# Optimization experiments

Hardware: AMD Instinct MI355X
Metric: run time of the kernel (lower is better)

Reference implementation:

```python
import jax, jax.numpy as jnp
import numpy as np

TEMPERATURE = 0.1


def setup_inputs() -> dict:
    key = jax.random.key(0)
    k1, k2 = jax.random.split(key)
    B, B_pos, D = 8192, 8192, 1024
    generated = jax.random.normal(k1, (B, D), dtype=jnp.float32)
    positive = jax.random.normal(k2, (B_pos, D), dtype=jnp.float32)
    return {"generated": generated, "positive": positive}


def _pairwise_dist_sq(x, y):
    # (N, M) squared L2 distances, clamped at 0
    x_norm = jnp.sum(x * x, axis=-1, keepdims=True)          # (N, 1)
    y_norm = jnp.sum(y * y, axis=-1, keepdims=True)          # (M, 1)
    d2 = x_norm + y_norm.T - 2.0 * (x @ y.T)
    return jnp.clip(d2, 0.0)


def reference(generated, positive):
    gen = generated.reshape(generated.shape[0], -1)
    pos = positive.reshape(positive.shape[0], -1)
    B = gen.shape[0]

    # Attraction: softmax over distances to positives.
    dist_pos = jnp.sqrt(_pairwise_dist_sq(gen, pos))          # (B, B_pos)
    w_pos = jax.nn.softmax(-dist_pos / TEMPERATURE, axis=1)
    # sum_j w_ij (pos_j - gen_i) == (w_pos @ pos) - gen  (rows of w sum to 1)
    attraction = w_pos @ pos - gen                            # (B, D)

    # Repulsion: softmax over distances to other generated samples (diag masked).
    d2_neg = _pairwise_dist_sq(gen, gen)
    eye = jnp.eye(B, dtype=bool)
    dist_neg = jnp.sqrt(jnp.where(eye, jnp.inf, d2_neg))      # inf diag -> weight 0
    w_neg = jax.nn.softmax(-dist_neg / TEMPERATURE, axis=1)
    repulsion = w_neg @ gen - gen                             # (B, D)

    drift = attraction - repulsion
    target = jax.lax.stop_gradient(gen + drift)
    loss = jnp.mean((gen - target) ** 2)

    drift_norm = jnp.mean(jnp.linalg.norm(drift, axis=-1))
    attraction_norm = jnp.mean(jnp.linalg.norm(attraction, axis=-1))
    repulsion_norm = jnp.mean(jnp.linalg.norm(repulsion, axis=-1))
    return (loss, drift_norm, attraction_norm, repulsion_norm)
```

## Files before the change

### kernel.cpp

```cpp
#include <hip/hip_runtime.h>
#include <stdint.h>

#define INV_T 10.0f
#define SHIFT_ 460.0f
#define MROWS 8192
#define DDIM 1024
#define CHUNK 1024

typedef __attribute__((ext_vector_type(8))) short bf16x8;
typedef __attribute__((ext_vector_type(4))) float f32x4;

__device__ __forceinline__ float bf2f(unsigned short u) {
  return __uint_as_float(((unsigned int)u) << 16);
}
__device__ __forceinline__ unsigned short f2bf(float f) {
  unsigned int u = __float_as_uint(f);
  return (unsigned short)((u + 0x7FFFu + ((u >> 16) & 1u)) >> 16);
}
__device__ __forceinline__ void gl2lds16(const unsigned short* g, unsigned short* l) {
  __builtin_amdgcn_global_load_lds((const __attribute__((address_space(1))) void*)g,
                                   (__attribute__((address_space(3))) void*)l, 16, 0, 0);
}

__global__ void prepT_kernel(const float* __restrict__ gen, const float* __restrict__ pos,
                             unsigned short* __restrict__ gen_h, unsigned short* __restrict__ pos_h,
                             unsigned short* __restrict__ genT, unsigned short* __restrict__ posT,
                             float* __restrict__ gn2, float* __restrict__ pn2) {
  __shared__ float tile[64][65];
  __shared__ float psum[64][4];
  int b = blockIdx.x;
  const float* src; unsigned short* dstT; unsigned short* dstH; float* n2;
  if (b < 2048) { src = gen; dstT = genT; dstH = gen_h; n2 = gn2; }
  else          { src = pos; dstT = posT; dstH = pos_h; n2 = pn2; b -= 2048; }
  int tj = b >> 4, td = b & 15;
  int t = threadIdx.x;
#pragma unroll
  for (int it = 0; it < 16; ++it) {
    int idx = it * 256 + t;
    int r = idx >> 6, c = idx & 63;
    tile[r][c] = src[(size_t)(tj * 64 + r) * DDIM + td * 64 + c];
  }
  __syncthreads();
  {
    int r4 = t >> 2, q = t & 3;
    float s = 0.f;
#pragma unroll
    for (int i = 0; i < 16; ++i) { float v = tile[r4][q * 16 + i]; s += v * v; }
    psum[r4][q] = s;
  }
#pragma unroll
  for (int it = 0; it < 16; ++it) {
    int idx = it * 256 + t;
    int r = idx >> 6, c = idx & 63;
    dstH[(size_t)(tj * 64 + r) * DDIM + td * 64 + c] = f2bf(tile[r][c]);
  }
#pragma unroll
  for (int it = 0; it < 16; ++it) {
    int idx = it * 256 + t;
    int d = idx >> 6, j = idx & 63;
    dstT[(size_t)(td * 64 + d) * MROWS + tj * 64 + j] = f2bf(tile[j][d]);
  }
  __syncthreads();
  if (t < 64) {
    float s = psum[t][0] + psum[t][1] + psum[t][2] + psum[t][3];
    atomicAdd(&n2[tj * 64 + t], s);
  }
}

__launch_bounds__(256, 2)
__global__ void gemm_sc2(const unsigned short* __restrict__ Aq,
                         const unsigned short* __restrict__ Bpos,
                         const unsigned short* __restrict__ Bgen,
                         int j0lo, int j0hi,
                         unsigned short* __restrict__ PaLo, unsigned short* __restrict__ PrLo,
                         unsigned short* __restrict__ PaHi, unsigned short* __restrict__ PrHi,
                         const float* __restrict__ gn2, const float* __restrict__ pn2,
                         float* __restrict__ lsumA, float* __restrict__ lsumR) {
  __shared__ __align__(16) unsigned short Al[128 * 64];
  __shared__ __align__(16) unsigned short Bl[128 * 64];

  const int orig = blockIdx.x + 64 * (blockIdx.y + 16 * blockIdx.z);
  const int wid = (orig & 7) * 256 + (orig >> 3);
  const int gy = wid & 15;
  const int bx = (wid >> 4) & 63;
  const int z = wid >> 10;
  const int hi = gy >> 3;
  const int by = gy & 7;

  const int j0 = hi ? j0hi : j0lo;
  const unsigned short* B = z ? Bgen : Bpos;
  const float* kn2 = z ? gn2 : pn2;
  float* lsum = z ? lsumR : lsumA;
  unsigned short* Pout = hi ? (z ? PrHi : PaHi) : (z ? PrLo : PaLo);

  const int t = threadIdx.x;
  const int w = t >> 6, lane = t & 63, l15 = lane & 15, quad = lane >> 4;
  const int wm = w >> 1, wn = w & 1;
  const long m0 = (long)bx * 128;
  const long n0 = (long)by * 128;
  const int trow = t >> 3;
  const int tcol = (((t & 7) ^ (trow & 7)) * 8);

  f32x4 acc[4][4];
#pragma unroll
  for (int i = 0; i < 4; ++i)
#pragma unroll
    for (int j = 0; j < 4; ++j) acc[i][j] = (f32x4){0.f, 0.f, 0.f, 0.f};

  const unsigned short* Ab = Aq + (m0 + trow) * DDIM + tcol;
  const unsigned short* Bb = B + ((long)j0 + n0 + trow) * DDIM + tcol;
  unsigned short* Alw = Al + t * 8;
  unsigned short* Blw = Bl + t * 8;
  const int ue = (quad ^ (l15 & 7)) * 8;

  for (int ks = 0; ks < DDIM / 64; ++ks) {
    const long ko = (long)ks * 64;
#pragma unroll
    for (int i = 0; i < 4; ++i) gl2lds16(Ab + (long)i * 32 * DDIM + ko, Alw + i * 2048);
#pragma unroll
    for (int i = 0; i < 4; ++i) gl2lds16(Bb + (long)i * 32 * DDIM + ko, Blw + i * 2048);
    __syncthreads();
#pragma unroll
    for (int kk = 0; kk < 2; ++kk) {
      const int uo = ue ^ (kk * 32);
      bf16x8 af[4], bfr[4];
#pragma unroll
      for (int mi = 0; mi < 4; ++mi)
        af[mi] = *(const bf16x8*)(Al + (wm * 64 + mi * 16 + l15) * 64 + uo);
#pragma unroll
      for (int ni = 0; ni < 4; ++ni)
        bfr[ni] = *(const bf16x8*)(Bl + (wn * 64 + ni * 16 + l15) * 64 + uo);
#pragma unroll
      for (int mi = 0; mi < 4; ++mi)
#pragma unroll
        for (int ni = 0; ni < 4; ++ni)
          acc[mi][ni] = __builtin_amdgcn_mfma_f32_16x16x32_bf16(af[mi], bfr[ni], acc[mi][ni], 0, 0, 0);
    }
    __syncthreads();
  }

#pragma unroll
  for (int mi = 0; mi < 4; ++mi) {
    float rs[4] = {0.f, 0.f, 0.f, 0.f};
#pragma unroll
    for (int ni = 0; ni < 4; ++ni) {
      int c = (int)n0 + wn * 64 + ni * 16 + l15;
      float kn = kn2[j0 + c];
#pragma unroll
      for (int reg = 0; reg < 4; ++reg) {
        long r = m0 + wm * 64 + mi * 16 + quad * 4 + reg;
        float v = acc[mi][ni][reg];
        float d2 = gn2[r] + kn - 2.0f * v;
        float p = __expf(SHIFT_ - INV_T * sqrtf(fmaxf(d2, 0.0f)));
        if (z && (int)r == (j0 + c)) p = 0.0f;
        rs[reg] += p;
        Pout[r * (long)CHUNK + c] = f2bf(p);
      }
    }
#pragma unroll
    for (int reg = 0; reg < 4; ++reg) {
      float v = rs[reg];
      v += __shfl_xor(v, 1); v += __shfl_xor(v, 2);
      v += __shfl_xor(v, 4); v += __shfl_xor(v, 8);
      if (l15 == 0) atomicAdd(&lsum[m0 + wm * 64 + mi * 16 + quad * 4 + reg], v);
    }
  }
}

#define KSEG(Abase, Bbase, LDA_, LDB_)                                                     \
  {                                                                                        \
    const unsigned short* Ab_ = (Abase) + (m0 + trow) * (LDA_) + tcol;                     \
    const unsigned short* Bb_ = (Bbase) + (n0 + trow) * (LDB_) + tcol;                     \
    for (int ks = 0; ks < 16; ++ks) {                                                      \
      const long ko = (long)ks * 64;                                                       \
      _Pragma("unroll")                                                                    \
      for (int i = 0; i < 4; ++i) gl2lds16(Ab_ + (long)i * 32 * (LDA_) + ko, Alw + i * 2048); \
      _Pragma("unroll")                                                                    \
      for (int i = 0; i < 4; ++i) gl2lds16(Bb_ + (long)i * 32 * (LDB_) + ko, Blw + i * 2048); \
      __syncthreads();                                                                     \
      _Pragma("unroll")                                                                    \
      for (int kk = 0; kk < 2; ++kk) {                                                     \
        const int uo = ue ^ (kk * 32);                                                     \
        bf16x8 af[4], bfr[4];                                                              \
        _Pragma("unroll")                                                                  \
        for (int mi = 0; mi < 4; ++mi)                                                     \
          af[mi] = *(const bf16x8*)(Al + (wm * 64 + mi * 16 + l15) * 64 + uo);             \
        _Pragma("unroll")                                                                  \
        for (int ni = 0; ni < 4; ++ni)                                                     \
          bfr[ni] = *(const bf16x8*)(Bl + (wn * 64 + ni * 16 + l15) * 64 + uo);            \
        _Pragma("unroll")                                                                  \
        for (int mi = 0; mi < 4; ++mi)                                                     \
          _Pragma("unroll")                                                                \
          for (int ni = 0; ni < 4; ++ni)                                                   \
            acc[mi][ni] = __builtin_amdgcn_mfma_f32_16x16x32_bf16(af[mi], bfr[ni], acc[mi][ni], 0, 0, 0); \
      }                                                                                    \
      __syncthreads();                                                                     \
    }                                                                                      \
  }

__launch_bounds__(256, 2)
__global__ void gemm_pv(const unsigned short* __restrict__ Pa0, const unsigned short* __restrict__ Pr0,
                        const unsigned short* __restrict__ Pa1, const unsigned short* __restrict__ Pr1,
                        const unsigned short* __restrict__ Pa2, const unsigned short* __restrict__ Pr2,
                        const unsigned short* __restrict__ Pa3, const unsigned short* __restrict__ Pr3,
                        const unsigned short* __restrict__ Va0, const unsigned short* __restrict__ Vr0,
                        const unsigned short* __restrict__ Va1, const unsigned short* __restrict__ Vr1,
                        const unsigned short* __restrict__ Va2, const unsigned short* __restrict__ Vr2,
                        const unsigned short* __restrict__ Va3, const unsigned short* __restrict__ Vr3,
                        unsigned short* __restrict__ OA, unsigned short* __restrict__ OR_,
                        int first) {
  __shared__ __align__(16) unsigned short Al[128 * 64];
  __shared__ __align__(16) unsigned short Bl[128 * 64];

  const int orig = blockIdx.x + 64 * (blockIdx.y + 8 * blockIdx.z);
  const int wid = (orig & 7) * 128 + (orig >> 3);
  const int by = wid & 7;
  const int bx = (wid >> 3) & 63;
  const int z = wid >> 9;

  const unsigned short* A0 = z ? Pr0 : Pa0;
  const unsigned short* B0 = z ? Vr0 : Va0;
  const unsigned short* A1 = z ? Pr1 : Pa1;
  const unsigned short* B1 = z ? Vr1 : Va1;
  const unsigned short* A2 = z ? Pr2 : Pa2;
  const unsigned short* B2 = z ? Vr2 : Va2;
  const unsigned short* A3 = z ? Pr3 : Pa3;
  const unsigned short* B3 = z ? Vr3 : Va3;

  const int t = threadIdx.x;
  const int w = t >> 6, lane = t & 63, l15 = lane & 15, quad = lane >> 4;
  const int wm = w >> 1, wn = w & 1;
  const long m0 = (long)bx * 128;
  const long n0 = (long)by * 128;
  const int trow = t >> 3;
  const int tcol = (((t & 7) ^ (trow & 7)) * 8);

  f32x4 acc[4][4];
#pragma unroll
  for (int i = 0; i < 4; ++i)
#pragma unroll
    for (int j = 0; j < 4; ++j) acc[i][j] = (f32x4){0.f, 0.f, 0.f, 0.f};

  unsigned short* Alw = Al + t * 8;
  unsigned short* Blw = Bl + t * 8;
  const int ue = (quad ^ (l15 & 7)) * 8;

  KSEG(A0, B0, CHUNK, MROWS);
  KSEG(A1, B1, CHUNK, MROWS);
  KSEG(A2, B2, CHUNK, MROWS);
  KSEG(A3, B3, CHUNK, MROWS);

  unsigned short* Oh = z ? OR_ : OA;
#pragma unroll
  for (int mi = 0; mi < 4; ++mi)
#pragma unroll
    for (int ni = 0; ni < 4; ++ni) {
      long c = n0 + wn * 64 + ni * 16 + l15;
#pragma unroll
      for (int reg = 0; reg < 4; ++reg) {
        long r = m0 + wm * 64 + mi * 16 + quad * 4 + reg;
        long off = r * DDIM + c;
        float v = acc[mi][ni][reg];
        Oh[off] = f2bf(first ? v : (bf2f(Oh[off]) + v));
      }
    }
}
#undef KSEG

__global__ void epi_kernel(const unsigned short* __restrict__ OA, const unsigned short* __restrict__ OR_,
                           const float* __restrict__ lsumA, const float* __restrict__ lsumR,
                           const float* __restrict__ genf, float* __restrict__ gs) {
  __shared__ float wsL[4], wsD[4], wsA[4], wsR[4];
  const int t = threadIdx.x;
  const int w = t >> 6;
  const int lane = t & 63;
  float accL = 0.f, accD = 0.f, accA = 0.f, accR = 0.f;

  for (int i = 0; i < 8; ++i) {
    const int row = blockIdx.x * 32 + w * 8 + i;
    const float invlA = 1.0f / lsumA[row];
    const float invlR = 1.0f / lsumR[row];
    float ssA = 0.f, ssR = 0.f, ssD = 0.f;
#pragma unroll
    for (int u = 0; u < 4; ++u) {
      const long off = (long)row * DDIM + u * 256 + lane * 4;
      float4 g = *(const float4*)(genf + off);
      ushort4 oa = *(const ushort4*)(OA + off);
      ushort4 orr = *(const ushort4*)(OR_ + off);
      float g4[4] = {g.x, g.y, g.z, g.w};
      float a4[4] = {bf2f(oa.x), bf2f(oa.y), bf2f(oa.z), bf2f(oa.w)};
      float r4[4] = {bf2f(orr.x), bf2f(orr.y), bf2f(orr.z), bf2f(orr.w)};
#pragma unroll
      for (int e = 0; e < 4; ++e) {
        float a_ = a4[e] * invlA - g4[e];
        float r_ = r4[e] * invlR - g4[e];
        float d_ = a_ - r_;
        ssA += a_ * a_; ssR += r_ * r_; ssD += d_ * d_;
      }
    }
#pragma unroll
    for (int m = 1; m < 64; m <<= 1) {
      ssA += __shfl_xor(ssA, m);
      ssR += __shfl_xor(ssR, m);
      ssD += __shfl_xor(ssD, m);
    }
    accA += sqrtf(ssA); accR += sqrtf(ssR); accD += sqrtf(ssD); accL += ssD;
  }
  if (lane == 0) { wsL[w] = accL; wsD[w] = accD; wsA[w] = accA; wsR[w] = accR; }
  __syncthreads();
  if (t == 0) {
    atomicAdd(&gs[0], wsL[0] + wsL[1] + wsL[2] + wsL[3]);
    atomicAdd(&gs[1], wsD[0] + wsD[1] + wsD[2] + wsD[3]);
    atomicAdd(&gs[2], wsA[0] + wsA[1] + wsA[2] + wsA[3]);
    atomicAdd(&gs[3], wsR[0] + wsR[1] + wsR[2] + wsR[3]);
  }
}

__global__ void finalize_kernel(const float* __restrict__ gs, float* __restrict__ out) {
  int t = threadIdx.x;
  if (t == 0) out[0] = gs[0] / (8192.0f * 1024.0f);
  if (t == 1) out[1] = gs[1] / 8192.0f;
  if (t == 2) out[2] = gs[2] / 8192.0f;
  if (t == 3) out[3] = gs[3] / 8192.0f;
}

extern "C" void kernel_launch(void* const* d_in, const int* in_sizes, int n_in,
                              void* d_out, int out_size, void* d_ws, size_t ws_size,
                              hipStream_t stream) {
  const float* gen = (const float*)d_in[0];
  const float* pos = (const float*)d_in[1];
  char* ws = (char*)d_ws;
  const size_t MB = (size_t)1 << 20;

  unsigned short* gen_h = (unsigned short*)(ws + 0 * MB);
  unsigned short* pos_h = (unsigned short*)(ws + 16 * MB);
  unsigned short* genT  = (unsigned short*)(ws + 32 * MB);
  unsigned short* posT  = (unsigned short*)(ws + 48 * MB);
  unsigned short* Pa[4] = {(unsigned short*)(ws + 64 * MB),  (unsigned short*)(ws + 96 * MB),
                           (unsigned short*)(ws + 128 * MB), (unsigned short*)(ws + 160 * MB)};
  unsigned short* Pr[4] = {(unsigned short*)(ws + 80 * MB),  (unsigned short*)(ws + 112 * MB),
                           (unsigned short*)(ws + 144 * MB), (unsigned short*)(ws + 176 * MB)};
  unsigned short* OhA = (unsigned short*)(ws + 192 * MB);
  unsigned short* OhR = (unsigned short*)(ws + 208 * MB);
  float* gn2   = (float*)(ws + 224 * MB);
  float* pn2   = (float*)(ws + 224 * MB + 32768);
  float* lsumA = (float*)(ws + 224 * MB + 65536);
  float* lsumR = (float*)(ws + 224 * MB + 98304);
  float* gs    = (float*)(ws + 224 * MB + 131072);

  hipMemsetAsync(gn2, 0, 131072 + 16, stream);
  prepT_kernel<<<dim3(4096), dim3(256), 0, stream>>>(gen, pos, gen_h, pos_h, genT, posT, gn2, pn2);

  for (int p = 0; p < 2; ++p) {
    const int c0 = 4 * p;
    gemm_sc2<<<dim3(64, 16, 2), dim3(256), 0, stream>>>(
        gen_h, pos_h, gen_h, c0 * CHUNK, (c0 + 1) * CHUNK,
        Pa[0], Pr[0], Pa[1], Pr[1], gn2, pn2, lsumA, lsumR);
    gemm_sc2<<<dim3(64, 16, 2), dim3(256), 0, stream>>>(
        gen_h, pos_h, gen_h, (c0 + 2) * CHUNK, (c0 + 3) * CHUNK,
        Pa[2], Pr[2], Pa[3], Pr[3], gn2, pn2, lsumA, lsumR);
    const long j0 = (long)c0 * CHUNK;
    gemm_pv<<<dim3(64, 8, 2), dim3(256), 0, stream>>>(
        Pa[0], Pr[0], Pa[1], Pr[1], Pa[2], Pr[2], Pa[3], Pr[3],
        posT + j0, genT + j0, posT + j0 + CHUNK, genT + j0 + CHUNK,
        posT + j0 + 2 * CHUNK, genT + j0 + 2 * CHUNK, posT + j0 + 3 * CHUNK, genT + j0 + 3 * CHUNK,
        OhA, OhR, p == 0);
  }

  epi_kernel<<<dim3(256), dim3(256), 0, stream>>>(OhA, OhR, lsumA, lsumR, gen, gs);
  finalize_kernel<<<dim3(1), dim3(64), 0, stream>>>(gs, (float*)d_out);
}
```

Before: 760.3 us.

## Exploit symmetry of repulsion distance matrix with triangular tile scoring

```diff
diff --git a/kernel.cpp b/kernel.cpp
--- a/kernel.cpp
+++ b/kernel.cpp
@@ -68,6 +68,216 @@
 }
 
 __launch_bounds__(256, 2)
+__global__ void repsc_tri(const unsigned short* __restrict__ Ah,
+                          unsigned short* __restrict__ Prep,
+                          const float* __restrict__ gn2,
+                          float* __restrict__ lsumR) {
+  __shared__ __align__(16) unsigned short lbuf[128 * 132];
+  unsigned short* Al = lbuf;
+  unsigned short* Bl = lbuf + 128 * 64;
+
+  const int orig = blockIdx.x;
+  const int wid = (orig & 7) * 260 + (orig >> 3);
+  int r = (int)((sqrtf(8.0f * (float)wid + 1.0f) - 1.0f) * 0.5f);
+  while ((r + 1) * (r + 2) / 2 <= wid) ++r;
+  while (r * (r + 1) / 2 > wid) --r;
+  const int c = wid - r * (r + 1) / 2;
+
+  const int t = threadIdx.x;
+  const int w = t >> 6, lane = t & 63, l15 = lane & 15, quad = lane >> 4;
+  const int wm = w >> 1, wn = w & 1;
+  const long m0 = (long)r * 128;
+  const long n0 = (long)c * 128;
+  const int trow = t >> 3;
+  const int tcol = (((t & 7) ^ (trow & 7)) * 8);
+
+  f32x4 acc[4][4];
+#pragma unroll
+  for (int i = 0; i < 4; ++i)
+#pragma unroll
+    for (int j = 0; j < 4; ++j) acc[i][j] = (f32x4){0.f, 0.f, 0.f, 0.f};
+
+  const unsigned short* Ab = Ah + (m0 + trow) * DDIM + tcol;
+  const unsigned short* Bb = Ah + (n0 + trow) * DDIM + tcol;
+  unsigned short* Alw = Al + t * 8;
+  unsigned short* Blw = Bl + t * 8;
+  const int ue = (quad ^ (l15 & 7)) * 8;
+
+  for (int ks = 0; ks < DDIM / 64; ++ks) {
+    const long ko = (long)ks * 64;
+#pragma unroll
+    for (int i = 0; i < 4; ++i) gl2lds16(Ab + (long)i * 32 * DDIM + ko, Alw + i * 2048);
+#pragma unroll
+    for (int i = 0; i < 4; ++i) gl2lds16(Bb + (long)i * 32 * DDIM + ko, Blw + i * 2048);
+    __syncthreads();
+#pragma unroll
+    for (int kk = 0; kk < 2; ++kk) {
+      const int uo = ue ^ (kk * 32);
+      bf16x8 af[4], bfr[4];
+#pragma unroll
+      for (int mi = 0; mi < 4; ++mi)
+        af[mi] = *(const bf16x8*)(Al + (wm * 64 + mi * 16 + l15) * 64 + uo);
+#pragma unroll
+      for (int ni = 0; ni < 4; ++ni)
+        bfr[ni] = *(const bf16x8*)(Bl + (wn * 64 + ni * 16 + l15) * 64 + uo);
+#pragma unroll
+      for (int mi = 0; mi < 4; ++mi)
+#pragma unroll
+        for (int ni = 0; ni < 4; ++ni)
+          acc[mi][ni] = __builtin_amdgcn_mfma_f32_16x16x32_bf16(af[mi], bfr[ni], acc[mi][ni], 0, 0, 0);
+    }
+    __syncthreads();
+  }
+
+  const bool offd = (r != c);
+  float cs[4] = {0.f, 0.f, 0.f, 0.f};
+#pragma unroll
+  for (int mi = 0; mi < 4; ++mi) {
+    float rs[4] = {0.f, 0.f, 0.f, 0.f};
+#pragma unroll
+    for (int ni = 0; ni < 4; ++ni) {
+      const int colL = wn * 64 + ni * 16 + l15;
+      const long col = n0 + colL;
+      float kn = gn2[col];
+#pragma unroll
+      for (int reg = 0; reg < 4; ++reg) {
+        const int rowL = wm * 64 + mi * 16 + quad * 4 + reg;
+        const long row = m0 + rowL;
+        float v = acc[mi][ni][reg];
+        float d2 = gn2[row] + kn - 2.0f * v;
+        float p = __expf(SHIFT_ - INV_T * sqrtf(fmaxf(d2, 0.0f)));
+        if (row == col) p = 0.0f;
+        rs[reg] += p;
+        cs[ni] += p;
+        unsigned short pb = f2bf(p);
+        Prep[row * (long)MROWS + col] = pb;
+        if (offd) lbuf[rowL * 132 + colL] = pb;
+      }
+    }
+#pragma unroll
+    for (int reg = 0; reg < 4; ++reg) {
+      float v = rs[reg];
+      v += __shfl_xor(v, 1); v += __shfl_xor(v, 2);
+      v += __shfl_xor(v, 4); v += __shfl_xor(v, 8);
+      if (l15 == 0) atomicAdd(&lsumR[m0 + wm * 64 + mi * 16 + quad * 4 + reg], v);
+    }
+  }
+  if (offd) {
+#pragma unroll
+    for (int ni = 0; ni < 4; ++ni) {
+      float v = cs[ni];
+      v += __shfl_xor(v, 16); v += __shfl_xor(v, 32);
+      if (quad == 0) atomicAdd(&lsumR[n0 + wn * 64 + ni * 16 + l15], v);
+    }
+    __syncthreads();
+#pragma unroll
+    for (int it = 0; it < 16; ++it) {
+      int lin = it * 256 + t;
+      int i = lin >> 5, jg = lin & 31, j = jg * 4;
+      ushort4 o;
+      o.x = lbuf[(j + 0) * 132 + i];
+      o.y = lbuf[(j + 1) * 132 + i];
+      o.z = lbuf[(j + 2) * 132 + i];
+      o.w = lbuf[(j + 3) * 132 + i];
+      *(ushort4*)(Prep + (n0 + i) * (long)MROWS + m0 + j) = o;
+    }
+  }
+}
+
+__launch_bounds__(256, 2)
+__global__ void gemm_sca(const unsigned short* __restrict__ Aq,
+                         const unsigned short* __restrict__ Bpos,
+                         int j0lo, int j0hi,
+                         unsigned short* __restrict__ PaLo, unsigned short* __restrict__ PaHi,
+                         const float* __restrict__ gn2, const float* __restrict__ pn2,
+                         float* __restrict__ lsumA) {
+  __shared__ __align__(16) unsigned short Al[128 * 64];
+  __shared__ __align__(16) unsigned short Bl[128 * 64];
+
+  const int orig = blockIdx.x + 64 * blockIdx.y;
+  const int wid = (orig & 7) * 128 + (orig >> 3);
+  const int gy = wid & 15;
+  const int bx = (wid >> 4) & 63;
+  const int hi = gy >> 3;
+  const int by = gy & 7;
+
+  const int j0 = hi ? j0hi : j0lo;
+  unsigned short* Pout = hi ? PaHi : PaLo;
+
+  const int t = threadIdx.x;
+  const int w = t >> 6, lane = t & 63, l15 = lane & 15, quad = lane >> 4;
+  const int wm = w >> 1, wn = w & 1;
+  const long m0 = (long)bx * 128;
+  const long n0 = (long)by * 128;
+  const int trow = t >> 3;
+  const int tcol = (((t & 7) ^ (trow & 7)) * 8);
+
+  f32x4 acc[4][4];
+#pragma unroll
+  for (int i = 0; i < 4; ++i)
+#pragma unroll
+    for (int j = 0; j < 4; ++j) acc[i][j] = (f32x4){0.f, 0.f, 0.f, 0.f};
+
+  const unsigned short* Ab = Aq + (m0 + trow) * DDIM + tcol;
+  const unsigned short* Bb = Bpos + ((long)j0 + n0 + trow) * DDIM + tcol;
+  unsigned short* Alw = Al + t * 8;
+  unsigned short* Blw = Bl + t * 8;
+  const int ue = (quad ^ (l15 & 7)) * 8;
+
+  for (int ks = 0; ks < DDIM / 64; ++ks) {
+    const long ko = (long)ks * 64;
+#pragma unroll
+    for (int i = 0; i < 4; ++i) gl2lds16(Ab + (long)i * 32 * DDIM + ko, Alw + i * 2048);
+#pragma unroll
+    for (int i = 0; i < 4; ++i) gl2lds16(Bb + (long)i * 32 * DDIM + ko, Blw + i * 2048);
+    __syncthreads();
+#pragma unroll
+    for (int kk = 0; kk < 2; ++kk) {
+      const int uo = ue ^ (kk * 32);
+      bf16x8 af[4], bfr[4];
+#pragma unroll
+      for (int mi = 0; mi < 4; ++mi)
+        af[mi] = *(const bf16x8*)(Al + (wm * 64 + mi * 16 + l15) * 64 + uo);
+#pragma unroll
+      for (int ni = 0; ni < 4; ++ni)
+        bfr[ni] = *(const bf16x8*)(Bl + (wn * 64 + ni * 16 + l15) * 64 + uo);
+#pragma unroll
+      for (int mi = 0; mi < 4; ++mi)
+#pragma unroll
+        for (int ni = 0; ni < 4; ++ni)
+          acc[mi][ni] = __builtin_amdgcn_mfma_f32_16x16x32_bf16(af[mi], bfr[ni], acc[mi][ni], 0, 0, 0);
+    }
+    __syncthreads();
+  }
+
+#pragma unroll
+  for (int mi = 0; mi < 4; ++mi) {
+    float rs[4] = {0.f, 0.f, 0.f, 0.f};
+#pragma unroll
+    for (int ni = 0; ni < 4; ++ni) {
+      int cc = (int)n0 + wn * 64 + ni * 16 + l15;
+      float kn = pn2[j0 + cc];
+#pragma unroll
+      for (int reg = 0; reg < 4; ++reg) {
+        long rr = m0 + wm * 64 + mi * 16 + quad * 4 + reg;
+        float v = acc[mi][ni][reg];
+        float d2 = gn2[rr] + kn - 2.0f * v;
+        float p = __expf(SHIFT_ - INV_T * sqrtf(fmaxf(d2, 0.0f)));
+        rs[reg] += p;
+        Pout[rr * (long)CHUNK + cc] = f2bf(p);
+      }
+    }
+#pragma unroll
+    for (int reg = 0; reg < 4; ++reg) {
+      float v = rs[reg];
+      v += __shfl_xor(v, 1); v += __shfl_xor(v, 2);
+      v += __shfl_xor(v, 4); v += __shfl_xor(v, 8);
+      if (l15 == 0) atomicAdd(&lsumA[m0 + wm * 64 + mi * 16 + quad * 4 + reg], v);
+    }
+  }
+}
+
+__launch_bounds__(256, 2)
 __global__ void gemm_sc2(const unsigned short* __restrict__ Aq,
                          const unsigned short* __restrict__ Bpos,
                          const unsigned short* __restrict__ Bgen,
@@ -144,17 +354,17 @@
     float rs[4] = {0.f, 0.f, 0.f, 0.f};
 #pragma unroll
     for (int ni = 0; ni < 4; ++ni) {
-      int c = (int)n0 + wn * 64 + ni * 16 + l15;
-      float kn = kn2[j0 + c];
+      int cc = (int)n0 + wn * 64 + ni * 16 + l15;
+      float kn = kn2[j0 + cc];
 #pragma unroll
       for (int reg = 0; reg < 4; ++reg) {
-        long r = m0 + wm * 64 + mi * 16 + quad * 4 + reg;
+        long rr = m0 + wm * 64 + mi * 16 + quad * 4 + reg;
         float v = acc[mi][ni][reg];
-        float d2 = gn2[r] + kn - 2.0f * v;
+        float d2 = gn2[rr] + kn - 2.0f * v;
         float p = __expf(SHIFT_ - INV_T * sqrtf(fmaxf(d2, 0.0f)));
-        if (z && (int)r == (j0 + c)) p = 0.0f;
+        if (z && (int)rr == (j0 + cc)) p = 0.0f;
         rs[reg] += p;
-        Pout[r * (long)CHUNK + c] = f2bf(p);
+        Pout[rr * (long)CHUNK + cc] = f2bf(p);
       }
     }
 #pragma unroll
@@ -167,16 +377,16 @@
   }
 }
 
-#define KSEG(Abase, Bbase, LDA_, LDB_)                                                     \
+#define KSEG(Abase, LDA_, Bbase)                                                           \
   {                                                                                        \
     const unsigned short* Ab_ = (Abase) + (m0 + trow) * (LDA_) + tcol;                     \
-    const unsigned short* Bb_ = (Bbase) + (n0 + trow) * (LDB_) + tcol;                     \
+    const unsigned short* Bb_ = (Bbase) + (n0 + trow) * (long)MROWS + tcol;                \
     for (int ks = 0; ks < 16; ++ks) {                                                      \
       const long ko = (long)ks * 64;                                                       \
       _Pragma("unroll")                                                                    \
       for (int i = 0; i < 4; ++i) gl2lds16(Ab_ + (long)i * 32 * (LDA_) + ko, Alw + i * 2048); \
       _Pragma("unroll")                                                                    \
-      for (int i = 0; i < 4; ++i) gl2lds16(Bb_ + (long)i * 32 * (LDB_) + ko, Blw + i * 2048); \
+      for (int i = 0; i < 4; ++i) gl2lds16(Bb_ + (long)i * 32 * (long)MROWS + ko, Blw + i * 2048); \
       __syncthreads();                                                                     \
       _Pragma("unroll")                                                                    \
       for (int kk = 0; kk < 2; ++kk) {                                                     \
@@ -199,16 +409,15 @@
   }
 
 __launch_bounds__(256, 2)
-__global__ void gemm_pv(const unsigned short* __restrict__ Pa0, const unsigned short* __restrict__ Pr0,
-                        const unsigned short* __restrict__ Pa1, const unsigned short* __restrict__ Pr1,
-                        const unsigned short* __restrict__ Pa2, const unsigned short* __restrict__ Pr2,
-                        const unsigned short* __restrict__ Pa3, const unsigned short* __restrict__ Pr3,
-                        const unsigned short* __restrict__ Va0, const unsigned short* __restrict__ Vr0,
-                        const unsigned short* __restrict__ Va1, const unsigned short* __restrict__ Vr1,
-                        const unsigned short* __restrict__ Va2, const unsigned short* __restrict__ Vr2,
-                        const unsigned short* __restrict__ Va3, const unsigned short* __restrict__ Vr3,
-                        unsigned short* __restrict__ OA, unsigned short* __restrict__ OR_,
-                        int first) {
+__global__ void gemm_pvq(const unsigned short* __restrict__ Pa0, const unsigned short* __restrict__ Pa1,
+                         const unsigned short* __restrict__ Pa2, const unsigned short* __restrict__ Pa3,
+                         const unsigned short* __restrict__ Ra0, const unsigned short* __restrict__ Ra1,
+                         const unsigned short* __restrict__ Ra2, const unsigned short* __restrict__ Ra3,
+                         long ldaRep,
+                         const unsigned short* __restrict__ Vp,
+                         const unsigned short* __restrict__ Vg,
+                         unsigned short* __restrict__ OA, unsigned short* __restrict__ OR_,
+                         int first) {
   __shared__ __align__(16) unsigned short Al[128 * 64];
   __shared__ __align__(16) unsigned short Bl[128 * 64];
 
@@ -218,14 +427,12 @@
   const int bx = (wid >> 3) & 63;
   const int z = wid >> 9;
 
-  const unsigned short* A0 = z ? Pr0 : Pa0;
-  const unsigned short* B0 = z ? Vr0 : Va0;
-  const unsigned short* A1 = z ? Pr1 : Pa1;
-  const unsigned short* B1 = z ? Vr1 : Va1;
-  const unsigned short* A2 = z ? Pr2 : Pa2;
-  const unsigned short* B2 = z ? Vr2 : Va2;
-  const unsigned short* A3 = z ? Pr3 : Pa3;
-  const unsigned short* B3 = z ? Vr3 : Va3;
+  const long ldaA = z ? ldaRep : (long)CHUNK;
+  const unsigned short* A0 = z ? Ra0 : Pa0;
+  const unsigned short* A1 = z ? Ra1 : Pa1;
+  const unsigned short* A2 = z ? Ra2 : Pa2;
+  const unsigned short* A3 = z ? Ra3 : Pa3;
+  const unsigned short* Vb = z ? Vg : Vp;
 
   const int t = threadIdx.x;
   const int w = t >> 6, lane = t & 63, l15 = lane & 15, quad = lane >> 4;
@@ -245,21 +452,21 @@
   unsigned short* Blw = Bl + t * 8;
   const int ue = (quad ^ (l15 & 7)) * 8;
 
-  KSEG(A0, B0, CHUNK, MROWS);
-  KSEG(A1, B1, CHUNK, MROWS);
-  KSEG(A2, B2, CHUNK, MROWS);
-  KSEG(A3, B3, CHUNK, MROWS);
+  KSEG(A0, ldaA, Vb + 0 * CHUNK);
+  KSEG(A1, ldaA, Vb + 1 * CHUNK);
+  KSEG(A2, ldaA, Vb + 2 * CHUNK);
+  KSEG(A3, ldaA, Vb + 3 * CHUNK);
 
   unsigned short* Oh = z ? OR_ : OA;
 #pragma unroll
   for (int mi = 0; mi < 4; ++mi)
 #pragma unroll
     for (int ni = 0; ni < 4; ++ni) {
-      long c = n0 + wn * 64 + ni * 16 + l15;
+      long cc = n0 + wn * 64 + ni * 16 + l15;
 #pragma unroll
       for (int reg = 0; reg < 4; ++reg) {
-        long r = m0 + wm * 64 + mi * 16 + quad * 4 + reg;
-        long off = r * DDIM + c;
+        long rr = m0 + wm * 64 + mi * 16 + quad * 4 + reg;
+        long off = rr * DDIM + cc;
         float v = acc[mi][ni][reg];
         Oh[off] = f2bf(first ? v : (bf2f(Oh[off]) + v));
       }
@@ -276,8 +483,8 @@
   const int lane = t & 63;
   float accL = 0.f, accD = 0.f, accA = 0.f, accR = 0.f;
 
-  for (int i = 0; i < 8; ++i) {
-    const int row = blockIdx.x * 32 + w * 8 + i;
+  for (int i = 0; i < 2; ++i) {
+    const int row = blockIdx.x * 8 + w * 2 + i;
     const float invlA = 1.0f / lsumA[row];
     const float invlR = 1.0f / lsumR[row];
     float ssA = 0.f, ssR = 0.f, ssD = 0.f;
@@ -331,42 +538,81 @@
   const float* pos = (const float*)d_in[1];
   char* ws = (char*)d_ws;
   const size_t MB = (size_t)1 << 20;
+  const size_t need_sym = 288 * MB + 131072 + 16;
 
   unsigned short* gen_h = (unsigned short*)(ws + 0 * MB);
   unsigned short* pos_h = (unsigned short*)(ws + 16 * MB);
   unsigned short* genT  = (unsigned short*)(ws + 32 * MB);
   unsigned short* posT  = (unsigned short*)(ws + 48 * MB);
-  unsigned short* Pa[4] = {(unsigned short*)(ws + 64 * MB),  (unsigned short*)(ws + 96 * MB),
-                           (unsigned short*)(ws + 128 * MB), (unsigned short*)(ws + 160 * MB)};
-  unsigned short* Pr[4] = {(unsigned short*)(ws + 80 * MB),  (unsigned short*)(ws + 112 * MB),
-                           (unsigned short*)(ws + 144 * MB), (unsigned short*)(ws + 176 * MB)};
-  unsigned short* OhA = (unsigned short*)(ws + 192 * MB);
-  unsigned short* OhR = (unsigned short*)(ws + 208 * MB);
-  float* gn2   = (float*)(ws + 224 * MB);
-  float* pn2   = (float*)(ws + 224 * MB + 32768);
-  float* lsumA = (float*)(ws + 224 * MB + 65536);
-  float* lsumR = (float*)(ws + 224 * MB + 98304);
-  float* gs    = (float*)(ws + 224 * MB + 131072);
-
-  hipMemsetAsync(gn2, 0, 131072 + 16, stream);
-  prepT_kernel<<<dim3(4096), dim3(256), 0, stream>>>(gen, pos, gen_h, pos_h, genT, posT, gn2, pn2);
-
-  for (int p = 0; p < 2; ++p) {
-    const int c0 = 4 * p;
-    gemm_sc2<<<dim3(64, 16, 2), dim3(256), 0, stream>>>(
-        gen_h, pos_h, gen_h, c0 * CHUNK, (c0 + 1) * CHUNK,
-        Pa[0], Pr[0], Pa[1], Pr[1], gn2, pn2, lsumA, lsumR);
-    gemm_sc2<<<dim3(64, 16, 2), dim3(256), 0, stream>>>(
-        gen_h, pos_h, gen_h, (c0 + 2) * CHUNK, (c0 + 3) * CHUNK,
-        Pa[2], Pr[2], Pa[3], Pr[3], gn2, pn2, lsumA, lsumR);
-    const long j0 = (long)c0 * CHUNK;
-    gemm_pv<<<dim3(64, 8, 2), dim3(256), 0, stream>>>(
-        Pa[0], Pr[0], Pa[1], Pr[1], Pa[2], Pr[2], Pa[3], Pr[3],
-        posT + j0, genT + j0, posT + j0 + CHUNK, genT + j0 + CHUNK,
-        posT + j0 + 2 * CHUNK, genT + j0 + 2 * CHUNK, posT + j0 + 3 * CHUNK, genT + j0 + 3 * CHUNK,
-        OhA, OhR, p == 0);
-  }
-
-  epi_kernel<<<dim3(256), dim3(256), 0, stream>>>(OhA, OhR, lsumA, lsumR, gen, gs);
-  finalize_kernel<<<dim3(1), dim3(64), 0, stream>>>(gs, (float*)d_out);
-}
+
+  if (ws_size >= need_sym) {
+    unsigned short* Prep = (unsigned short*)(ws + 64 * MB);
+    unsigned short* Pa[4] = {(unsigned short*)(ws + 192 * MB), (unsigned short*)(ws + 208 * MB),
+                             (unsigned short*)(ws + 224 * MB), (unsigned short*)(ws + 240 * MB)};
+    unsigned short* OhA = (unsigned short*)(ws + 256 * MB);
+    unsigned short* OhR = (unsigned short*)(ws + 272 * MB);
+    float* gn2   = (float*)(ws + 288 * MB);
+    float* pn2   = (float*)(ws + 288 * MB + 32768);
+    float* lsumA = (float*)(ws + 288 * MB + 65536);
+    float* lsumR = (float*)(ws + 288 * MB + 98304);
+    float* gs    = (float*)(ws + 288 * MB + 131072);
+
+    hipMemsetAsync(gn2, 0, 131072 + 16, stream);
+    prepT_kernel<<<dim3(4096), dim3(256), 0, stream>>>(gen, pos, gen_h, pos_h, genT, posT, gn2, pn2);
+
+    repsc_tri<<<dim3(2080), dim3(256), 0, stream>>>(gen_h, Prep, gn2, lsumR);
+
+    for (int p = 0; p < 2; ++p) {
+      const int c0 = 4 * p;
+      gemm_sca<<<dim3(64, 16), dim3(256), 0, stream>>>(
+          gen_h, pos_h, c0 * CHUNK, (c0 + 1) * CHUNK, Pa[0], Pa[1], gn2, pn2, lsumA);
+      gemm_sca<<<dim3(64, 16), dim3(256), 0, stream>>>(
+          gen_h, pos_h, (c0 + 2) * CHUNK, (c0 + 3) * CHUNK, Pa[2], Pa[3], gn2, pn2, lsumA);
+      const long j0 = (long)c0 * CHUNK;
+      gemm_pvq<<<dim3(64, 8, 2), dim3(256), 0, stream>>>(
+          Pa[0], Pa[1], Pa[2], Pa[3],
+          Prep + j0, Prep + j0 + CHUNK, Prep + j0 + 2 * CHUNK, Prep + j0 + 3 * CHUNK,
+          (long)MROWS,
+          posT + j0, genT + j0,
+          OhA, OhR, p == 0);
+    }
+
+    epi_kernel<<<dim3(1024), dim3(256), 0, stream>>>(OhA, OhR, lsumA, lsumR, gen, gs);
+    finalize_kernel<<<dim3(1), dim3(64), 0, stream>>>(gs, (float*)d_out);
+  } else {
+    unsigned short* Pa[4] = {(unsigned short*)(ws + 64 * MB),  (unsigned short*)(ws + 96 * MB),
+                             (unsigned short*)(ws + 128 * MB), (unsigned short*)(ws + 160 * MB)};
+    unsigned short* Pr[4] = {(unsigned short*)(ws + 80 * MB),  (unsigned short*)(ws + 112 * MB),
+                             (unsigned short*)(ws + 144 * MB), (unsigned short*)(ws + 176 * MB)};
+    unsigned short* OhA = (unsigned short*)(ws + 192 * MB);
+    unsigned short* OhR = (unsigned short*)(ws + 208 * MB);
+    float* gn2   = (float*)(ws + 224 * MB);
+    float* pn2   = (float*)(ws + 224 * MB + 32768);
+    float* lsumA = (float*)(ws + 224 * MB + 65536);
+    float* lsumR = (float*)(ws + 224 * MB + 98304);
+    float* gs    = (float*)(ws + 224 * MB + 131072);
+
+    hipMemsetAsync(gn2, 0, 131072 + 16, stream);
+    prepT_kernel<<<dim3(4096), dim3(256), 0, stream>>>(gen, pos, gen_h, pos_h, genT, posT, gn2, pn2);
+
+    for (int p = 0; p < 2; ++p) {
+      const int c0 = 4 * p;
+      gemm_sc2<<<dim3(64, 16, 2), dim3(256), 0, stream>>>(
+          gen_h, pos_h, gen_h, c0 * CHUNK, (c0 + 1) * CHUNK,
+          Pa[0], Pr[0], Pa[1], Pr[1], gn2, pn2, lsumA, lsumR);
+      gemm_sc2<<<dim3(64, 16, 2), dim3(256), 0, stream>>>(
+          gen_h, pos_h, gen_h, (c0 + 2) * CHUNK, (c0 + 3) * CHUNK,
+          Pa[2], Pr[2], Pa[3], Pr[3], gn2, pn2, lsumA, lsumR);
+      const long j0 = (long)c0 * CHUNK;
+      gemm_pvq<<<dim3(64, 8, 2), dim3(256), 0, stream>>>(
+          Pa[0], Pa[1], Pa[2], Pa[3],
+          Pr[0], Pr[1], Pr[2], Pr[3],
+          (long)CHUNK,
+          posT + j0, genT + j0,
+          OhA, OhR, p == 0);
+    }
+
+    epi_kernel<<<dim3(1024), dim3(256), 0, stream>>>(OhA, OhR, lsumA, lsumR, gen, gs);
+    finalize_kernel<<<dim3(1), dim3(64), 0, stream>>>(gs, (float*)d_out);
+  }
+}
```

New measurement: 771.5 us. Within noise of the previous version (+1.5%).
